# Performance work log

Measured on AMD Instinct MI355X. Metric: run time of the kernel, lower is better.

The kernel has to match this reference:

```python
import jax, jax.numpy as jnp
import numpy as np

N_HEAD = 16
CHUNK = 128  # block size for the causal linear-attention scan


def _phi(x):
    return jax.nn.elu(x) + 1.0


def setup_inputs() -> dict:
    key = jax.random.key(0)
    k1, k2, k3 = jax.random.split(key, 3)
    B, T, E = 4, 2048, 1024
    x = jax.random.normal(k1, (B, T, E), dtype=jnp.float32)
    w_attn = jax.random.normal(k2, (3 * E, E), dtype=jnp.float32) * 0.02
    w_proj = jax.random.normal(k3, (E, E), dtype=jnp.float32) * 0.02
    return {"x": x, "w_attn": w_attn, "w_proj": w_proj}


def _causal_linear_attn(qp, kp, v):
    # qp, kp, v: [B, H, T, D]; phi already applied to qp, kp
    B, H, T, D = qp.shape
    NC = T // CHUNK

    def to_chunks(a):  # -> [NC, B, H, CHUNK, D]
        return a.reshape(B, H, NC, CHUNK, D).transpose(2, 0, 1, 3, 4)

    qc, kc, vc = to_chunks(qp), to_chunks(kp), to_chunks(v)
    mask = jnp.tril(jnp.ones((CHUNK, CHUNK), dtype=bool))

    def step(carry, blk):
        S, z = carry  # S: [B,H,D,D] = sum_{prev} k v^T ; z: [B,H,D] = sum_{prev} k
        q_c, k_c, v_c = blk  # [B,H,CHUNK,D]
        scores = jnp.einsum('bhcd,bhkd->bhck', q_c, k_c)
        scores = jnp.where(mask, scores, 0.0)
        num = (jnp.einsum('bhck,bhke->bhce', scores, v_c)
               + jnp.einsum('bhcd,bhde->bhce', q_c, S))
        den = scores.sum(-1) + jnp.einsum('bhcd,bhd->bhc', q_c, z)
        S = S + jnp.einsum('bhkd,bhke->bhde', k_c, v_c)
        z = z + k_c.sum(axis=2)
        return (S, z), (num, den)

    S0 = jnp.zeros((B, H, D, D), dtype=qp.dtype)
    z0 = jnp.zeros((B, H, D), dtype=qp.dtype)
    _, (num, den) = jax.lax.scan(step, (S0, z0), (qc, kc, vc))
    y = num / (den[..., None] + 1e-6)  # [NC,B,H,CHUNK,D]
    y = y.transpose(1, 2, 0, 3, 4).reshape(B, H, T, D)
    return y


def reference(x, w_attn, w_proj):
    B, T, E = x.shape
    H = N_HEAD
    D = E // H
    qkv = x @ w_attn.T  # [B,T,3E]
    q, k, v = jnp.split(qkv, 3, axis=2)

    def heads(a):  # [B,T,E] -> [B,H,T,D]
        return a.reshape(B, T, H, D).transpose(0, 2, 1, 3)

    y = _causal_linear_attn(_phi(heads(q)), _phi(heads(k)), heads(v))
    y = y.transpose(0, 2, 1, 3).reshape(B, T, E)
    return y @ w_proj.T
```

## Files before the change

kernel.cpp:

```cpp
#include <hip/hip_runtime.h>
#include <math.h>

#define B_ 4
#define T_ 2048
#define E_ 1024
#define H_ 16
#define D_ 64
#define CHUNK_ 128
#define NC_ 16
#define BH_ (B_ * H_)
#define M_ (B_ * T_)

typedef __attribute__((ext_vector_type(8))) short bf16x8;
typedef __attribute__((ext_vector_type(4))) float f32x4;

__device__ __forceinline__ ushort rnbf(float f) {
  unsigned u = __float_as_uint(f);
  unsigned r = (u + 0x7FFFu + ((u >> 16) & 1u)) >> 16;
  return (ushort)r;
}

__device__ __forceinline__ float bf2f(short s) {
  return __uint_as_float(((unsigned)(ushort)s) << 16);
}

__device__ __forceinline__ void gload_lds16(const void* g, void* l) {
  __builtin_amdgcn_global_load_lds(
      (const __attribute__((address_space(1))) unsigned int*)g,
      (__attribute__((address_space(3))) unsigned int*)l, 16, 0, 0);
}

#define VMW(N) do { asm volatile("s_waitcnt vmcnt(" #N ")" ::: "memory"); \
                    __builtin_amdgcn_sched_barrier(0); } while (0)
#define BARR() do { __builtin_amdgcn_s_barrier(); \
                    __builtin_amdgcn_sched_barrier(0); } while (0)

#define N4X_ (M_ * E_ / 4)
#define N4A_ (3 * E_ * E_ / 4)
#define N4P_ (E_ * E_ / 4)
__global__ __launch_bounds__(256) void k_cvt3(
    const float* __restrict__ x, const float* __restrict__ wa,
    const float* __restrict__ wp, ushort* __restrict__ xb,
    ushort* __restrict__ wab, ushort* __restrict__ wpb) {
  int i = blockIdx.x * 256 + threadIdx.x;
  const float* src;
  ushort* dst;
  int off;
  if (i < N4X_) { src = x; dst = xb; off = i; }
  else if (i < N4X_ + N4A_) { src = wa; dst = wab; off = i - N4X_; }
  else { src = wp; dst = wpb; off = i - (N4X_ + N4A_); }
  float4 v = ((const float4*)src)[off];
  ushort4 o;
  o.x = rnbf(v.x); o.y = rnbf(v.y); o.z = rnbf(v.z); o.w = rnbf(v.w);
  ((ushort4*)dst)[off] = o;
}

#define STG(sl_, tt_) { \
  gload_lds16(Asrc + (tt_) * 32, &lds[(sl_) * 4096 + tid * 8]); \
  gload_lds16(Bsrc0 + (tt_) * 32, &lds[12288 + (sl_) * 8192 + tid * 8]); \
  gload_lds16(Bsrc1 + (tt_) * 32, &lds[12288 + (sl_) * 8192 + 4096 + tid * 8]); }

#define LDFRAGS(sl_) \
  const ushort* pa = &lds[(sl_) * 4096 + aOff]; \
  a0 = *(const bf16x8*)pa;          a1 = *(const bf16x8*)(pa + 512); \
  a2 = *(const bf16x8*)(pa + 1024); a3 = *(const bf16x8*)(pa + 1536); \
  const ushort* pb = &lds[12288 + (sl_) * 8192 + bOff]; \
  b0 = *(const bf16x8*)pb;          b1 = *(const bf16x8*)(pb + 512); \
  b2 = *(const bf16x8*)(pb + 1024); b3 = *(const bf16x8*)(pb + 1536);

#define MM(i, j, A_, B_) \
  acc[i][j] = __builtin_amdgcn_mfma_f32_16x16x32_bf16(A_, B_, acc[i][j], 0, 0, 0)
#define MFMA16() do { __builtin_amdgcn_s_setprio(1); \
  MM(0,0,a0,b0); MM(0,1,a0,b1); MM(0,2,a0,b2); MM(0,3,a0,b3); \
  MM(1,0,a1,b0); MM(1,1,a1,b1); MM(1,2,a1,b2); MM(1,3,a1,b3); \
  MM(2,0,a2,b0); MM(2,1,a2,b1); MM(2,2,a2,b2); MM(2,3,a2,b3); \
  MM(3,0,a3,b0); MM(3,1,a3,b1); MM(3,2,a3,b2); MM(3,3,a3,b3); \
  __builtin_amdgcn_s_setprio(0); } while (0)

__device__ __forceinline__ void pipe_gemm(const ushort* __restrict__ Ag,
                                          const ushort* __restrict__ Bg,
                                          ushort* lds, f32x4 acc[4][4]) {
  const int tid = threadIdx.x;
  const int l = tid & 63, wv = tid >> 6;
  const int wm = wv >> 2, wn = wv & 3;
  const int c16 = l & 15, g4 = l >> 4;
  const int gch = (tid & 3) ^ ((tid >> 3) & 3);
  const ushort* Asrc = Ag + (size_t)(tid >> 2) * 1024 + gch * 8;
  const ushort* Bsrc0 = Bg + (size_t)(tid >> 2) * 1024 + gch * 8;
  const ushort* Bsrc1 = Bsrc0 + (size_t)128 * 1024;
  const int xq = (c16 >> 1) & 3;
  const int aOff = (wm * 64 + c16) * 32 + ((g4 ^ xq) << 3);
  const int bOff = (wn * 64 + c16) * 32 + ((g4 ^ xq) << 3);

  STG(0, 0);
  STG(1, 1);
  int sl = 0;
#pragma unroll 3
  for (int t = 0; t < 30; ++t) {
    const int slN = sl ? sl - 1 : 2;
    VMW(3); BARR();
    bf16x8 a0, a1, a2, a3, b0, b1, b2, b3;
    LDFRAGS(sl);
    STG(slN, t + 2);
    MFMA16();
    sl = (sl == 2) ? 0 : sl + 1;
  }
  {
    VMW(3); BARR();
    bf16x8 a0, a1, a2, a3, b0, b1, b2, b3;
    LDFRAGS(0);
    MFMA16();
  }
  {
    VMW(0); BARR();
    bf16x8 a0, a1, a2, a3, b0, b1, b2, b3;
    LDFRAGS(1);
    MFMA16();
  }
}

__global__ __launch_bounds__(512, 4) void k_qkv2(
    const ushort* __restrict__ xb, const ushort* __restrict__ wab,
    ushort* __restrict__ qg, ushort* __restrict__ kg,
    ushort* __restrict__ ktg, ushort* __restrict__ vtg,
    float* __restrict__ zp) {
  extern __shared__ ushort lds[];
  const int b = blockIdx.x;
  const int xcd = b & 7, idx = b >> 3;
  const int bm = xcd * 8 + (idx & 7);
  const int bn = idx >> 3;
  const int tid = threadIdx.x;
  const int wv = tid >> 6, l = tid & 63;
  const int wm = wv >> 2, wn = wv & 3;
  const int c16 = l & 15, g4 = l >> 4;

  f32x4 acc[4][4] = {};
  pipe_gemm(xb + (size_t)bm * 128 * 1024, wab + (size_t)bn * 256 * 1024, lds, acc);

  BARR();
  const int colbase = bn * 256 + wn * 64;
  const int which = colbase >> 10;
  const int h = (colbase & 1023) >> 6;
  const int rowbase = bm * 128 + wm * 64;
  const int bidx = rowbase >> 11;
  const int tbase = rowbase & 2047;
  const size_t bh = (size_t)(bidx * 16 + h);
  ushort* wlds = &lds[wv * 4096];
  float zpart[4] = {0.f, 0.f, 0.f, 0.f};
#pragma unroll
  for (int mf = 0; mf < 4; ++mf) {
#pragma unroll
    for (int nf = 0; nf < 4; ++nf) {
      float o[4];
#pragma unroll
      for (int j = 0; j < 4; ++j) {
        float u = acc[mf][nf][j];
        o[j] = (which < 2) ? ((u > 0.f) ? u + 1.f : expf(u)) : u;
      }
      const int d = nf * 16 + c16;
      if (which == 1) zpart[nf] += o[0] + o[1] + o[2] + o[3];
      if (which <= 1) {
        ushort* dst = (which == 0) ? qg : kg;
        const size_t rb = (bh * 2048 + tbase + mf * 16 + g4 * 4) * 64 + d;
#pragma unroll
        for (int j = 0; j < 4; ++j) dst[rb + (size_t)j * 64] = rnbf(o[j]);
      }
      if (which >= 1) {
        const int tb = (mf * 4 + g4) ^ ((d & 3) << 1);
        ushort4 pk;
        pk.x = rnbf(o[0]); pk.y = rnbf(o[1]); pk.z = rnbf(o[2]); pk.w = rnbf(o[3]);
        *(ushort4*)&wlds[d * 64 + tb * 4] = pk;
      }
    }
  }
  if (which == 1) {
    const int cc = tbase >> 7;
#pragma unroll
    for (int nf = 0; nf < 4; ++nf) {
      float zz = zpart[nf];
      zz += __shfl_xor(zz, 16);
      zz += __shfl_xor(zz, 32);
      if (l < 16) zp[((bh * NC_ + cc) * 2 + wm) * 64 + nf * 16 + l] = zz;
    }
  }
  if (which >= 1) {
    asm volatile("s_waitcnt lgkmcnt(0)" ::: "memory");
    __builtin_amdgcn_sched_barrier(0);
    ushort* tg = (which == 1) ? ktg : vtg;
#pragma unroll
    for (int it = 0; it < 8; ++it) {
      const int d = it * 8 + (l >> 3);
      const int t0 = (l & 7) * 8;
      const int blk = ((l & 7) * 2) ^ ((d & 3) << 1);
      bf16x8 vv_ = *(const bf16x8*)&wlds[d * 64 + blk * 4];
      *(bf16x8*)&tg[(bh * 64 + d) * 2048 + tbase + t0] = vv_;
    }
  }
}

__global__ __launch_bounds__(512, 4) void k_proj2(
    const ushort* __restrict__ yb, const ushort* __restrict__ wpb,
    float* __restrict__ out) {
  extern __shared__ ushort lds[];
  const int b = blockIdx.x;
  const int xcd = b & 7, idx = b >> 3;
  const int bm = xcd * 8 + (idx & 7);
  const int bn = idx >> 3;
  const int tid = threadIdx.x;
  const int wv = tid >> 6, l = tid & 63;
  const int wm = wv >> 2, wn = wv & 3;
  const int c16 = l & 15, g4 = l >> 4;

  f32x4 acc[4][4] = {};
  pipe_gemm(yb + (size_t)bm * 128 * 1024, wpb + (size_t)bn * 256 * 1024, lds, acc);

  const int rowbase = bm * 128 + wm * 64 + g4 * 4;
  const int colbase = bn * 256 + wn * 64 + c16;
#pragma unroll
  for (int mf = 0; mf < 4; ++mf)
#pragma unroll
    for (int nf = 0; nf < 4; ++nf) {
      const size_t base = (size_t)(rowbase + mf * 16) * 1024 + colbase + nf * 16;
#pragma unroll
      for (int j = 0; j < 4; ++j)
        out[base + (size_t)j * 1024] = acc[mf][nf][j];
    }
}

__global__ __launch_bounds__(256) void k_stats(const ushort* __restrict__ ktg,
                                               const ushort* __restrict__ vtg,
                                               float* __restrict__ Sc) {
  __shared__ __align__(16) ushort kT_s[64 * 128], vT_s[64 * 128];
  const int blk = blockIdx.x;
  const int bh = blk >> 4, c = blk & 15;
  const int tid = threadIdx.x;
  const int w = tid >> 6, l = tid & 63;
  const ushort* ktb = ktg + (size_t)bh * D_ * T_ + c * CHUNK_;
  const ushort* vtb = vtg + (size_t)bh * D_ * T_ + c * CHUNK_;
#pragma unroll
  for (int s2 = 0; s2 < 4; ++s2) {
    const int seg = w * 4 + s2;
    const int row = seg * 4 + (l >> 4);
    const int sb = ((l & 15) ^ (row & 7)) * 8;
    gload_lds16(ktb + (size_t)row * T_ + sb, &kT_s[seg * 512]);
    gload_lds16(vtb + (size_t)row * T_ + sb, &vT_s[seg * 512]);
  }
  __syncthreads();
  const int wr = w >> 1, wc = w & 1;
  f32x4 acc[2][2] = {};
#pragma unroll
  for (int kt = 0; kt < 4; ++kt) {
    const int g = kt * 32 + (l >> 4) * 8;
    bf16x8 av[2], bk[2];
#pragma unroll
    for (int rt = 0; rt < 2; ++rt) {
      const int e = wr * 32 + rt * 16 + (l & 15);
      av[rt] = *(const bf16x8*)&vT_s[e * 128 + (g ^ ((e & 7) << 3))];
    }
#pragma unroll
    for (int ct = 0; ct < 2; ++ct) {
      const int d = wc * 32 + ct * 16 + (l & 15);
      bk[ct] = *(const bf16x8*)&kT_s[d * 128 + (g ^ ((d & 7) << 3))];
    }
#pragma unroll
    for (int rt = 0; rt < 2; ++rt)
#pragma unroll
      for (int ct = 0; ct < 2; ++ct)
        acc[rt][ct] = __builtin_amdgcn_mfma_f32_16x16x32_bf16(av[rt], bk[ct],
                                                              acc[rt][ct], 0, 0, 0);
  }
  float* So = Sc + (size_t)blk * 4096;
#pragma unroll
  for (int rt = 0; rt < 2; ++rt)
#pragma unroll
    for (int ct = 0; ct < 2; ++ct)
#pragma unroll
      for (int jj = 0; jj < 4; ++jj)
        So[(wr * 32 + rt * 16 + (l >> 4) * 4 + jj) * 64 + wc * 32 + ct * 16 + (l & 15)] =
            acc[rt][ct][jj];
}

__global__ __launch_bounds__(256) void k_prefix2(const float* __restrict__ Sc,
                                                 ushort* __restrict__ STb,
                                                 const float* __restrict__ zp,
                                                 float* __restrict__ zout) {
  const int b = blockIdx.x;
  const int tid = threadIdx.x;
  if (b < 256) {
    const int bh = b >> 2, qt = b & 3;
    const float4* Sb = (const float4*)(Sc + (size_t)bh * NC_ * 4096) + qt * 256 + tid;
    ushort4* Ob = (ushort4*)(STb + (size_t)bh * NC_ * 4096) + qt * 256 + tid;
    float4 v[16];
#pragma unroll
    for (int c = 0; c < NC_; ++c) v[c] = Sb[c * 1024];
    float4 acc = make_float4(0.f, 0.f, 0.f, 0.f);
#pragma unroll
    for (int c = 0; c < NC_; ++c) {
      ushort4 o;
      o.x = rnbf(acc.x); o.y = rnbf(acc.y); o.z = rnbf(acc.z); o.w = rnbf(acc.w);
      Ob[c * 1024] = o;
      acc.x += v[c].x; acc.y += v[c].y; acc.z += v[c].z; acc.w += v[c].w;
    }
  } else {
    const int bh = b - 256;
    if (tid < 16) {
      const float4* zpb = (const float4*)(zp + (size_t)bh * NC_ * 128);
      float4* zob = (float4*)(zout + (size_t)bh * NC_ * 64);
      float4 t0[16], t1[16];
#pragma unroll
      for (int c = 0; c < NC_; ++c) {
        t0[c] = zpb[c * 32 + tid];
        t1[c] = zpb[c * 32 + 16 + tid];
      }
      float4 za = make_float4(0.f, 0.f, 0.f, 0.f);
#pragma unroll
      for (int c = 0; c < NC_; ++c) {
        zob[c * 16 + tid] = za;
        za.x += t0[c].x + t1[c].x; za.y += t0[c].y + t1[c].y;
        za.z += t0[c].z + t1[c].z; za.w += t0[c].w + t1[c].w;
      }
    }
  }
}

__global__ __launch_bounds__(512, 4) void k_out(
    const ushort* __restrict__ qg, const ushort* __restrict__ kg,
    const ushort* __restrict__ vtg, const ushort* __restrict__ STb,
    const float* __restrict__ zg, ushort* __restrict__ yb) {
  __shared__ __align__(16) ushort k_s[128 * 64];
  __shared__ __align__(16) ushort vT_s[64 * 128];
  __shared__ __align__(16) ushort ST_s[64 * 64];
  __shared__ __align__(16) ushort P_s[128 * 128];
  __shared__ float z_s[64];
  __shared__ float dinter_s[128];
  const int blk = blockIdx.x;
  const int bh = blk >> 4, c = blk & 15;
  const int tid = threadIdx.x;
  const int w = tid >> 6, l = tid & 63;

  const ushort* kbase = kg + ((size_t)bh * T_ + c * CHUNK_) * D_;
  const ushort* vbase = vtg + (size_t)bh * D_ * T_ + c * CHUNK_;
  const ushort* sbase = STb + ((size_t)bh * NC_ + c) * 4096;
  {
    int seg = w, row = seg * 8 + (l >> 3);
    gload_lds16(kbase + (size_t)row * 64 + ((l & 7) ^ (row & 7)) * 8, &k_s[seg * 512]);
    seg = w + 8; row = seg * 8 + (l >> 3);
    gload_lds16(kbase + (size_t)row * 64 + ((l & 7) ^ (row & 7)) * 8, &k_s[seg * 512]);
  }
  {
    int seg = w, row = seg * 4 + (l >> 4);
    gload_lds16(vbase + (size_t)row * T_ + ((l & 15) ^ (row & 7)) * 8, &vT_s[seg * 512]);
    seg = w + 8; row = seg * 4 + (l >> 4);
    gload_lds16(vbase + (size_t)row * T_ + ((l & 15) ^ (row & 7)) * 8, &vT_s[seg * 512]);
  }
  {
    const int seg = w, row = seg * 8 + (l >> 3);
    gload_lds16(sbase + (size_t)row * 64 + ((l & 7) ^ (row & 7)) * 8, &ST_s[seg * 512]);
  }
  if (tid < 64) z_s[tid] = zg[((size_t)bh * NC_ + c) * 64 + tid];
  const int arow = w * 16 + (l & 15);
  const ushort* qrow = qg + ((size_t)bh * T_ + c * CHUNK_ + arow) * D_ + (l >> 4) * 8;
  bf16x8 qf0 = *(const bf16x8*)(qrow);
  bf16x8 qf1 = *(const bf16x8*)(qrow + 32);
  __syncthreads();

  f32x4 sc[8] = {};
#pragma unroll
  for (int jt = 0; jt < 8; ++jt) {
    const int j = jt * 16 + (l & 15);
    const int sw = (j & 7) << 3, g = (l >> 4) * 8;
    bf16x8 b0 = *(const bf16x8*)&k_s[j * 64 + (g ^ sw)];
    bf16x8 b1 = *(const bf16x8*)&k_s[j * 64 + ((g + 32) ^ sw)];
    sc[jt] = __builtin_amdgcn_mfma_f32_16x16x32_bf16(qf0, b0, sc[jt], 0, 0, 0);
    sc[jt] = __builtin_amdgcn_mfma_f32_16x16x32_bf16(qf1, b1, sc[jt], 0, 0, 0);
  }
  const int crow0 = w * 16 + (l >> 4) * 4;
  float rsum[4] = {0.f, 0.f, 0.f, 0.f};
#pragma unroll
  for (int jt = 0; jt < 8; ++jt) {
    const int j = jt * 16 + (l & 15);
#pragma unroll
    for (int jj = 0; jj < 4; ++jj) {
      const int i = crow0 + jj;
      float s = (j <= i) ? sc[jt][jj] : 0.f;
      rsum[jj] += s;
      P_s[i * 128 + (j ^ ((i & 7) << 3))] = rnbf(s);
    }
  }
  float di = 0.f;
#pragma unroll
  for (int jj = 0; jj < 8; ++jj) {
    di = fmaf(bf2f(qf0[jj]), z_s[(l >> 4) * 8 + jj], di);
    di = fmaf(bf2f(qf1[jj]), z_s[32 + (l >> 4) * 8 + jj], di);
  }
  di += __shfl_xor(di, 16);
  di += __shfl_xor(di, 32);
  if (l < 16) dinter_s[w * 16 + l] = di;
#pragma unroll
  for (int jj = 0; jj < 4; ++jj) {
    float r = rsum[jj];
    r += __shfl_xor(r, 1); r += __shfl_xor(r, 2);
    r += __shfl_xor(r, 4); r += __shfl_xor(r, 8);
    rsum[jj] = r;
  }
  __syncthreads();

  f32x4 acc2[4] = {};
#pragma unroll
  for (int et = 0; et < 4; ++et) {
    const int e = et * 16 + (l & 15);
    const int sw = (e & 7) << 3, g = (l >> 4) * 8;
    bf16x8 s0 = *(const bf16x8*)&ST_s[e * 64 + (g ^ sw)];
    bf16x8 s1 = *(const bf16x8*)&ST_s[e * 64 + ((g + 32) ^ sw)];
    acc2[et] = __builtin_amdgcn_mfma_f32_16x16x32_bf16(qf0, s0, acc2[et], 0, 0, 0);
    acc2[et] = __builtin_amdgcn_mfma_f32_16x16x32_bf16(qf1, s1, acc2[et], 0, 0, 0);
  }
  const int prow = w * 16 + (l & 15);
  const int psw = (prow & 7) << 3;
#pragma unroll
  for (int jkt = 0; jkt < 4; ++jkt) {
    bf16x8 pa = *(const bf16x8*)&P_s[prow * 128 + ((jkt * 32 + (l >> 4) * 8) ^ psw)];
#pragma unroll
    for (int et = 0; et < 4; ++et) {
      const int e = et * 16 + (l & 15);
      bf16x8 bv = *(const bf16x8*)&vT_s[e * 128 +
                                        ((jkt * 32 + (l >> 4) * 8) ^ ((e & 7) << 3))];
      acc2[et] = __builtin_amdgcn_mfma_f32_16x16x32_bf16(pa, bv, acc2[et], 0, 0, 0);
    }
  }
  float inv[4];
#pragma unroll
  for (int jj = 0; jj < 4; ++jj)
    inv[jj] = 1.0f / (rsum[jj] + dinter_s[crow0 + jj] + 1e-6f);
  const int b = bh >> 4, h = bh & 15;
#pragma unroll
  for (int et = 0; et < 4; ++et) {
    const int d = et * 16 + (l & 15);
#pragma unroll
    for (int jj = 0; jj < 4; ++jj) {
      const int t = c * CHUNK_ + crow0 + jj;
      yb[((size_t)(b * T_ + t) * H_ + h) * D_ + d] = rnbf(acc2[et][jj] * inv[jj]);
    }
  }
}

extern "C" void kernel_launch(void* const* d_in, const int* in_sizes, int n_in,
                              void* d_out, int out_size, void* d_ws, size_t ws_size,
                              hipStream_t stream) {
  const float* x = (const float*)d_in[0];
  const float* w_attn = (const float*)d_in[1];
  const float* w_proj = (const float*)d_in[2];
  float* out = (float*)d_out;

  ushort* xb = (ushort*)d_ws;
  ushort* wab = xb + (size_t)M_ * E_;
  ushort* wpb = wab + (size_t)3 * E_ * E_;
  ushort* qb = wpb + (size_t)E_ * E_;
  ushort* kbm = qb + (size_t)M_ * E_;
  ushort* kT = kbm + (size_t)M_ * E_;
  ushort* vT = kT + (size_t)M_ * E_;
  ushort* yb = vT + (size_t)M_ * E_;
  ushort* STb = yb + (size_t)M_ * E_;
  float* Schunk = (float*)(STb + (size_t)BH_ * NC_ * 4096);
  float* zpart = Schunk + (size_t)BH_ * NC_ * 4096;
  float* zout = zpart + (size_t)BH_ * NC_ * 2 * 64;

  k_cvt3<<<12288, 256, 0, stream>>>(x, w_attn, w_proj, xb, wab, wpb);

  hipFuncSetAttribute((const void*)k_qkv2,
                      hipFuncAttributeMaxDynamicSharedMemorySize, 73728);
  hipFuncSetAttribute((const void*)k_proj2,
                      hipFuncAttributeMaxDynamicSharedMemorySize, 73728);

  k_qkv2<<<768, 512, 73728, stream>>>(xb, wab, qb, kbm, kT, vT, zpart);
  k_stats<<<1024, 256, 0, stream>>>(kT, vT, Schunk);
  k_prefix2<<<320, 256, 0, stream>>>(Schunk, STb, zpart, zout);
  k_out<<<1024, 512, 0, stream>>>(qb, kbm, vT, STb, zout, yb);
  k_proj2<<<256, 512, 73728, stream>>>(yb, wpb, out);
}
```

Baseline: 128.8 us.

## Shrink GEMM pipeline to double buffering and transpose epilogue in halves to cut LDS

The shared GEMM mainloop moves from a three-slot to a two-slot LDS ring, with an extra barrier before each stage is refilled. The k/v transpose epilogue in k_qkv2 now runs in two 32-row halves through a smaller swizzled LDS scratch. Together these lower dynamic LDS from 72 KB to 48 KB, and k_qkv2's launch bound is raised to 6 blocks to allow higher occupancy. In exchange, the next tile's loads are only issued after the MFMAs finish, so global-to-LDS prefetch overlaps compute less, and each iteration carries an extra barrier.

```diff
diff --git a/kernel.cpp b/kernel.cpp
--- a/kernel.cpp
+++ b/kernel.cpp
@@ -33,6 +33,8 @@
 #define VMW(N) do { asm volatile("s_waitcnt vmcnt(" #N ")" ::: "memory"); \
                     __builtin_amdgcn_sched_barrier(0); } while (0)
 #define BARR() do { __builtin_amdgcn_s_barrier(); \
+                    __builtin_amdgcn_sched_barrier(0); } while (0)
+#define LGK0() do { asm volatile("s_waitcnt lgkmcnt(0)" ::: "memory"); \
                     __builtin_amdgcn_sched_barrier(0); } while (0)
 
 #define N4X_ (M_ * E_ / 4)
@@ -55,16 +57,19 @@
   ((ushort4*)dst)[off] = o;
 }
 
+#define ABASE(sl_) ((sl_) * 4096)
+#define BBASE(sl_) (8192 + (sl_) * 8192)
+
 #define STG(sl_, tt_) { \
-  gload_lds16(Asrc + (tt_) * 32, &lds[(sl_) * 4096 + tid * 8]); \
-  gload_lds16(Bsrc0 + (tt_) * 32, &lds[12288 + (sl_) * 8192 + tid * 8]); \
-  gload_lds16(Bsrc1 + (tt_) * 32, &lds[12288 + (sl_) * 8192 + 4096 + tid * 8]); }
+  gload_lds16(Asrc + (tt_) * 32, &lds[ABASE(sl_) + tid * 8]); \
+  gload_lds16(Bsrc0 + (tt_) * 32, &lds[BBASE(sl_) + tid * 8]); \
+  gload_lds16(Bsrc1 + (tt_) * 32, &lds[BBASE(sl_) + tid * 8 + 4096]); }
 
 #define LDFRAGS(sl_) \
-  const ushort* pa = &lds[(sl_) * 4096 + aOff]; \
+  const ushort* pa = &lds[ABASE(sl_) + aOff]; \
   a0 = *(const bf16x8*)pa;          a1 = *(const bf16x8*)(pa + 512); \
   a2 = *(const bf16x8*)(pa + 1024); a3 = *(const bf16x8*)(pa + 1536); \
-  const ushort* pb = &lds[12288 + (sl_) * 8192 + bOff]; \
+  const ushort* pb = &lds[BBASE(sl_) + bOff]; \
   b0 = *(const bf16x8*)pb;          b1 = *(const bf16x8*)(pb + 512); \
   b2 = *(const bf16x8*)(pb + 1024); b3 = *(const bf16x8*)(pb + 1536);
 
@@ -94,16 +99,15 @@
 
   STG(0, 0);
   STG(1, 1);
-  int sl = 0;
-#pragma unroll 3
+#pragma unroll 2
   for (int t = 0; t < 30; ++t) {
-    const int slN = sl ? sl - 1 : 2;
+    const int sl = t & 1;
     VMW(3); BARR();
     bf16x8 a0, a1, a2, a3, b0, b1, b2, b3;
     LDFRAGS(sl);
-    STG(slN, t + 2);
     MFMA16();
-    sl = (sl == 2) ? 0 : sl + 1;
+    BARR();
+    STG(sl, t + 2);
   }
   {
     VMW(3); BARR();
@@ -119,7 +123,7 @@
   }
 }
 
-__global__ __launch_bounds__(512, 4) void k_qkv2(
+__global__ __launch_bounds__(512, 6) void k_qkv2(
     const ushort* __restrict__ xb, const ushort* __restrict__ wab,
     ushort* __restrict__ qg, ushort* __restrict__ kg,
     ushort* __restrict__ ktg, ushort* __restrict__ vtg,
@@ -145,32 +149,54 @@
   const int bidx = rowbase >> 11;
   const int tbase = rowbase & 2047;
   const size_t bh = (size_t)(bidx * 16 + h);
-  ushort* wlds = &lds[wv * 4096];
+  ushort* wlds2 = &lds[8192 + wv * 2048];
+  ushort* tg = (which == 1) ? ktg : vtg;
   float zpart[4] = {0.f, 0.f, 0.f, 0.f};
 #pragma unroll
-  for (int mf = 0; mf < 4; ++mf) {
-#pragma unroll
-    for (int nf = 0; nf < 4; ++nf) {
-      float o[4];
-#pragma unroll
-      for (int j = 0; j < 4; ++j) {
-        float u = acc[mf][nf][j];
-        o[j] = (which < 2) ? ((u > 0.f) ? u + 1.f : expf(u)) : u;
+  for (int p = 0; p < 2; ++p) {
+#pragma unroll
+    for (int mh = 0; mh < 2; ++mh) {
+      const int mf = p * 2 + mh;
+#pragma unroll
+      for (int nf = 0; nf < 4; ++nf) {
+        float o[4];
+#pragma unroll
+        for (int j = 0; j < 4; ++j) {
+          float u = acc[mf][nf][j];
+          o[j] = (which < 2) ? ((u > 0.f) ? u + 1.f : expf(u)) : u;
+        }
+        const int d = nf * 16 + c16;
+        if (which == 1) zpart[nf] += o[0] + o[1] + o[2] + o[3];
+        if (which <= 1) {
+          ushort* dst = (which == 0) ? qg : kg;
+          const size_t rb = (bh * 2048 + tbase + mf * 16 + g4 * 4) * 64 + d;
+#pragma unroll
+          for (int j = 0; j < 4; ++j) dst[rb + (size_t)j * 64] = rnbf(o[j]);
+        }
+        if (which >= 1) {
+          const int tb2 = (mh * 4 + g4) ^ (d & 7);
+          ushort4 pk;
+          pk.x = rnbf(o[0]); pk.y = rnbf(o[1]); pk.z = rnbf(o[2]); pk.w = rnbf(o[3]);
+          *(ushort4*)&wlds2[d * 32 + tb2 * 4] = pk;
+        }
       }
-      const int d = nf * 16 + c16;
-      if (which == 1) zpart[nf] += o[0] + o[1] + o[2] + o[3];
-      if (which <= 1) {
-        ushort* dst = (which == 0) ? qg : kg;
-        const size_t rb = (bh * 2048 + tbase + mf * 16 + g4 * 4) * 64 + d;
-#pragma unroll
-        for (int j = 0; j < 4; ++j) dst[rb + (size_t)j * 64] = rnbf(o[j]);
+    }
+    if (which >= 1) {
+      LGK0();
+#pragma unroll
+      for (int rt = 0; rt < 4; ++rt) {
+        const int d = rt * 16 + (l >> 2);
+        const int t0 = (l & 3) * 8;
+        const int ba = ((l & 3) * 2) ^ (d & 7);
+        const int bb = ((l & 3) * 2 + 1) ^ (d & 7);
+        ushort4 ua = *(const ushort4*)&wlds2[d * 32 + ba * 4];
+        ushort4 ub = *(const ushort4*)&wlds2[d * 32 + bb * 4];
+        __align__(16) ushort tmp[8] = {ua.x, ua.y, ua.z, ua.w,
+                                       ub.x, ub.y, ub.z, ub.w};
+        *(bf16x8*)&tg[(bh * 64 + d) * 2048 + tbase + p * 32 + t0] =
+            *(const bf16x8*)tmp;
       }
-      if (which >= 1) {
-        const int tb = (mf * 4 + g4) ^ ((d & 3) << 1);
-        ushort4 pk;
-        pk.x = rnbf(o[0]); pk.y = rnbf(o[1]); pk.z = rnbf(o[2]); pk.w = rnbf(o[3]);
-        *(ushort4*)&wlds[d * 64 + tb * 4] = pk;
-      }
+      LGK0();
     }
   }
   if (which == 1) {
@@ -181,19 +207,6 @@
       zz += __shfl_xor(zz, 16);
       zz += __shfl_xor(zz, 32);
       if (l < 16) zp[((bh * NC_ + cc) * 2 + wm) * 64 + nf * 16 + l] = zz;
-    }
-  }
-  if (which >= 1) {
-    asm volatile("s_waitcnt lgkmcnt(0)" ::: "memory");
-    __builtin_amdgcn_sched_barrier(0);
-    ushort* tg = (which == 1) ? ktg : vtg;
-#pragma unroll
-    for (int it = 0; it < 8; ++it) {
-      const int d = it * 8 + (l >> 3);
-      const int t0 = (l & 7) * 8;
-      const int blk = ((l & 7) * 2) ^ ((d & 3) << 1);
-      bf16x8 vv_ = *(const bf16x8*)&wlds[d * 64 + blk * 4];
-      *(bf16x8*)&tg[(bh * 64 + d) * 2048 + tbase + t0] = vv_;
     }
   }
 }
@@ -468,13 +481,13 @@
   k_cvt3<<<12288, 256, 0, stream>>>(x, w_attn, w_proj, xb, wab, wpb);
 
   hipFuncSetAttribute((const void*)k_qkv2,
-                      hipFuncAttributeMaxDynamicSharedMemorySize, 73728);
+                      hipFuncAttributeMaxDynamicSharedMemorySize, 49152);
   hipFuncSetAttribute((const void*)k_proj2,
-                      hipFuncAttributeMaxDynamicSharedMemorySize, 73728);
-
-  k_qkv2<<<768, 512, 73728, stream>>>(xb, wab, qb, kbm, kT, vT, zpart);
+                      hipFuncAttributeMaxDynamicSharedMemorySize, 49152);
+
+  k_qkv2<<<768, 512, 49152, stream>>>(xb, wab, qb, kbm, kT, vT, zpart);
   k_stats<<<1024, 256, 0, stream>>>(kT, vT, Schunk);
   k_prefix2<<<320, 256, 0, stream>>>(Schunk, STb, zpart, zout);
   k_out<<<1024, 512, 0, stream>>>(qb, kbm, vT, STb, zout, yb);
-  k_proj2<<<256, 512, 73728, stream>>>(yb, wpb, out);
-}
+  k_proj2<<<256, 512, 49152, stream>>>(yb, wpb, out);
+}
```

New measurement: 513.7 us. +298.8%, slower.
